# Kernel tuning notes

Hardware: AMD Instinct MI355X
Metric: run time of the kernel (lower is better)

The kernel has to match this reference:

```python
import jax, jax.numpy as jnp
import numpy as np

N_NODES = 50000
N_EDGES = 600000
HIDDEN = 128


def _sage_conv(x, src, dst, W_l, W_r, b):
    """PyG SAGEConv with mean aggregation:
    out_i = W_l @ mean_{j in N(i)} x_j + W_r @ x_i + b
    src/dst: [E] edge endpoints (message flows src -> dst).
    """
    msg = x[src]  # [E, d] gather
    agg = jax.ops.segment_sum(msg, dst, num_segments=N_NODES)  # [N, d]
    cnt = jax.ops.segment_sum(jnp.ones((src.shape[0],), x.dtype), dst,
                              num_segments=N_NODES)  # [N]
    mean = agg / jnp.maximum(cnt, 1.0)[:, None]
    return mean @ W_l.T + x @ W_r.T + b


def setup_inputs() -> dict:
    key = jax.random.key(0)
    ks = jax.random.split(key, 12)
    x = jax.random.normal(ks[0], (N_NODES, HIDDEN), dtype=jnp.float32)
    edge_index = jax.random.randint(ks[1], (2, N_EDGES), 0, N_NODES, dtype=jnp.int64)
    scale = 1.0 / np.sqrt(HIDDEN)
    inp = {"x": x, "edge_index": edge_index}
    for i, layer in enumerate(["1", "2", "3"]):
        inp["Wl" + layer] = jax.random.uniform(ks[2 + 3 * i], (HIDDEN, HIDDEN),
                                               minval=-scale, maxval=scale, dtype=jnp.float32)
        inp["Wr" + layer] = jax.random.uniform(ks[3 + 3 * i], (HIDDEN, HIDDEN),
                                               minval=-scale, maxval=scale, dtype=jnp.float32)
        inp["b" + layer] = jax.random.uniform(ks[4 + 3 * i], (HIDDEN,),
                                              minval=-scale, maxval=scale, dtype=jnp.float32)
    return inp


def reference(x, edge_index, Wl1, Wr1, b1, Wl2, Wr2, b2, Wl3, Wr3, b3):
    src, dst = edge_index[0], edge_index[1]
    h = jax.nn.relu(_sage_conv(x, src, dst, Wl1, Wr1, b1))
    h = _sage_conv(h, src, dst, Wl2, Wr2, b2)
    h = _sage_conv(h, src, dst, Wl3, Wr3, b3)
    return h
```

## Files before the change

kernel.cpp:

```cpp
#include <hip/hip_runtime.h>
#include <hip/hip_bf16.h>

#define N_NODES 50000
#define N_EDGES 600000
#define HID 128

typedef __attribute__((ext_vector_type(8))) short s8v;
typedef __attribute__((ext_vector_type(8))) unsigned short u8v;
typedef __attribute__((ext_vector_type(4))) float f4v;

__device__ __forceinline__ unsigned short f2bf(float x) {
    unsigned u = __float_as_uint(x);
    unsigned r = u + 0x7FFFu + ((u >> 16) & 1u);
    return (unsigned short)(r >> 16);
}
__device__ __forceinline__ float bf2f(unsigned short u) {
    return __uint_as_float((unsigned)u << 16);
}
__device__ __forceinline__ void split_bf(float x, unsigned short& hi, unsigned short& lo) {
    hi = f2bf(x);
    lo = f2bf(x - bf2f(hi));
}

__global__ void detect_mode(const void* __restrict__ edges, int* __restrict__ flag) {
    __shared__ int any;
    if (threadIdx.x == 0) any = 0;
    __syncthreads();
    const int* p = (const int*)edges;
    if (p[2 * threadIdx.x + 1] != 0) any = 1;
    __syncthreads();
    if (threadIdx.x == 0) *flag = (any == 0) ? 1 : 0;
}

__device__ __forceinline__ int edge_at(const void* edges, int mode64, long long idx) {
    return mode64 ? (int)((const long long*)edges)[idx] : ((const int*)edges)[idx];
}

__global__ void count_deg(const void* __restrict__ edges, const int* __restrict__ flag,
                          int* __restrict__ deg) {
    int e = blockIdx.x * 256 + threadIdx.x;
    if (e >= N_EDGES) return;
    int m = *flag;
    int d = edge_at(edges, m, (long long)N_EDGES + e);
    if ((unsigned)d < (unsigned)N_NODES) atomicAdd(&deg[d], 1);
}

__global__ void scan_block(const int* __restrict__ deg, int* __restrict__ offs,
                           int* __restrict__ blocksum) {
    __shared__ int sm[256];
    int i = blockIdx.x * 256 + threadIdx.x;
    int v = (i < N_NODES) ? deg[i] : 0;
    sm[threadIdx.x] = v;
    __syncthreads();
    #pragma unroll
    for (int s = 1; s < 256; s <<= 1) {
        int t = (threadIdx.x >= (unsigned)s) ? sm[threadIdx.x - s] : 0;
        __syncthreads();
        sm[threadIdx.x] += t;
        __syncthreads();
    }
    if (i < N_NODES) offs[i] = sm[threadIdx.x] - v;
    if (threadIdx.x == 255) blocksum[blockIdx.x] = sm[255];
}

__global__ void scan_top(int* __restrict__ blocksum, int nblocks) {
    __shared__ int sm[256];
    int v = ((int)threadIdx.x < nblocks) ? blocksum[threadIdx.x] : 0;
    sm[threadIdx.x] = v;
    __syncthreads();
    #pragma unroll
    for (int s = 1; s < 256; s <<= 1) {
        int t = (threadIdx.x >= (unsigned)s) ? sm[threadIdx.x - s] : 0;
        __syncthreads();
        sm[threadIdx.x] += t;
        __syncthreads();
    }
    if ((int)threadIdx.x < nblocks) blocksum[threadIdx.x] = sm[threadIdx.x] - v;
    if (threadIdx.x == 255) blocksum[nblocks] = sm[255];
}

__global__ void scan_add(int* __restrict__ offs, int* __restrict__ cursor,
                         const int* __restrict__ blocksum, int nblocks) {
    int i = blockIdx.x * 256 + threadIdx.x;
    if (i < N_NODES) {
        int o = offs[i] + blocksum[blockIdx.x];
        offs[i] = o;
        cursor[i] = o;
    }
    if (i == 0) offs[N_NODES] = blocksum[nblocks];
}

__global__ void fill_csr(const void* __restrict__ edges, const int* __restrict__ flag,
                         int* __restrict__ cursor, int* __restrict__ csr) {
    int e = blockIdx.x * 256 + threadIdx.x;
    if (e >= N_EDGES) return;
    int m = *flag;
    int d = edge_at(edges, m, (long long)N_EDGES + e);
    int s = edge_at(edges, m, (long long)e);
    if ((unsigned)d >= (unsigned)N_NODES || (unsigned)s >= (unsigned)N_NODES) return;
    int pos = atomicAdd(&cursor[d], 1);
    csr[pos] = s;
}

__global__ void convert_w(const float* __restrict__ m0, const float* __restrict__ m1,
                          const float* __restrict__ m2, const float* __restrict__ m3,
                          const float* __restrict__ m4, const float* __restrict__ m5,
                          unsigned short* __restrict__ whi, unsigned short* __restrict__ wlo) {
    int idx = blockIdx.x * 256 + threadIdx.x;
    if (idx >= 6 * HID * HID) return;
    int mat = idx >> 14, off = idx & 16383;
    const float* src = mat == 0 ? m0 : mat == 1 ? m1 : mat == 2 ? m2
                     : mat == 3 ? m3 : mat == 4 ? m4 : m5;
    unsigned short h, l;
    split_bf(src[off], h, l);
    whi[idx] = h; wlo[idx] = l;
}

__global__ void split_f32(const float* __restrict__ x, unsigned short* __restrict__ hi,
                          unsigned short* __restrict__ lo, int n4) {
    int i = blockIdx.x * 256 + threadIdx.x;
    if (i >= n4) return;
    float4 v = ((const float4*)x)[i];
    ushort4 h, l;
    split_bf(v.x, h.x, l.x);
    split_bf(v.y, h.y, l.y);
    split_bf(v.z, h.z, l.z);
    split_bf(v.w, h.w, l.w);
    ((ushort4*)hi)[i] = h;
    ((ushort4*)lo)[i] = l;
}

__global__ __launch_bounds__(256) void aggregate_bf16(const unsigned short* __restrict__ h,
                                                      const int* __restrict__ offs,
                                                      const int* __restrict__ csr,
                                                      unsigned short* __restrict__ mhi,
                                                      unsigned short* __restrict__ mlo) {
    const int sub  = threadIdx.x & 15;
    const int node = blockIdx.x * 16 + (threadIdx.x >> 4);
    if (node >= N_NODES) return;
    const int beg = offs[node], end = offs[node + 1];
    float a[8] = {0.f, 0.f, 0.f, 0.f, 0.f, 0.f, 0.f, 0.f};
    int p = beg;
    for (; p + 8 <= end; p += 8) {
        int s0 = csr[p],     s1 = csr[p + 1], s2 = csr[p + 2], s3 = csr[p + 3];
        int s4 = csr[p + 4], s5 = csr[p + 5], s6 = csr[p + 6], s7 = csr[p + 7];
        u8v v0 = *(const u8v*)(h + (size_t)s0 * HID + sub * 8);
        u8v v1 = *(const u8v*)(h + (size_t)s1 * HID + sub * 8);
        u8v v2 = *(const u8v*)(h + (size_t)s2 * HID + sub * 8);
        u8v v3 = *(const u8v*)(h + (size_t)s3 * HID + sub * 8);
        u8v v4 = *(const u8v*)(h + (size_t)s4 * HID + sub * 8);
        u8v v5 = *(const u8v*)(h + (size_t)s5 * HID + sub * 8);
        u8v v6 = *(const u8v*)(h + (size_t)s6 * HID + sub * 8);
        u8v v7 = *(const u8v*)(h + (size_t)s7 * HID + sub * 8);
        #pragma unroll
        for (int j = 0; j < 8; ++j)
            a[j] += ((bf2f(v0[j]) + bf2f(v1[j])) + (bf2f(v2[j]) + bf2f(v3[j])))
                  + ((bf2f(v4[j]) + bf2f(v5[j])) + (bf2f(v6[j]) + bf2f(v7[j])));
    }
    if (p + 4 <= end) {
        int s0 = csr[p], s1 = csr[p + 1], s2 = csr[p + 2], s3 = csr[p + 3];
        u8v v0 = *(const u8v*)(h + (size_t)s0 * HID + sub * 8);
        u8v v1 = *(const u8v*)(h + (size_t)s1 * HID + sub * 8);
        u8v v2 = *(const u8v*)(h + (size_t)s2 * HID + sub * 8);
        u8v v3 = *(const u8v*)(h + (size_t)s3 * HID + sub * 8);
        #pragma unroll
        for (int j = 0; j < 8; ++j)
            a[j] += (bf2f(v0[j]) + bf2f(v1[j])) + (bf2f(v2[j]) + bf2f(v3[j]));
        p += 4;
    }
    for (; p < end; ++p) {
        int s = csr[p];
        u8v v = *(const u8v*)(h + (size_t)s * HID + sub * 8);
        #pragma unroll
        for (int j = 0; j < 8; ++j) a[j] += bf2f(v[j]);
    }
    const float inv = 1.0f / fmaxf((float)(end - beg), 1.0f);
    u8v hh, ll;
    #pragma unroll
    for (int j = 0; j < 8; ++j) {
        unsigned short hj, lj;
        split_bf(a[j] * inv, hj, lj);
        hh[j] = hj; ll[j] = lj;
    }
    *(u8v*)(mhi + (size_t)node * HID + sub * 8) = hh;
    *(u8v*)(mlo + (size_t)node * HID + sub * 8) = ll;
}

template <int RELU, int FINAL>
__global__ __launch_bounds__(256) void sage_mfma(
    const unsigned short* __restrict__ Mhi, const unsigned short* __restrict__ Mlo,
    const unsigned short* __restrict__ Hhi, const unsigned short* __restrict__ Hlo,
    const unsigned short* __restrict__ Whi, const unsigned short* __restrict__ Wlo,
    const float* __restrict__ bias,
    unsigned short* __restrict__ ohi, unsigned short* __restrict__ olo,
    float* __restrict__ of32) {
    __shared__ short BhS[128 * 72];
    __shared__ short BlS[128 * 72];
    const int tid = threadIdx.x;
    const int wave = tid >> 6, lane = tid & 63;
    const int mIdx = lane & 15, q = lane >> 4;
    const int wrow = (wave & 1) * 64, wcol = (wave >> 1) * 64;
    const int rowBase = blockIdx.x * 128;

    size_t aoff[4];
    #pragma unroll
    for (int t = 0; t < 4; ++t) {
        int node = rowBase + wrow + t * 16 + mIdx;
        if (node > N_NODES - 1) node = N_NODES - 1;
        aoff[t] = (size_t)node * HID + q * 8;
    }

    const int bcol = tid & 127;
    const int bseg = (tid >> 7) * 32;

    f4v acc[4][4];
    #pragma unroll
    for (int a = 0; a < 4; ++a)
        #pragma unroll
        for (int b = 0; b < 4; ++b) acc[a][b] = (f4v){0.f, 0.f, 0.f, 0.f};

    s8v Ah[2][4], Al[2][4];
    auto loadA = [&](int i, int buf) {
        const unsigned short* ah_ = (i < 4) ? Mhi : Hhi;
        const unsigned short* al_ = (i < 4) ? Mlo : Hlo;
        const int kc = (i & 3) * 32;
        #pragma unroll
        for (int t = 0; t < 4; ++t) {
            Ah[buf][t] = *(const s8v*)(ah_ + aoff[t] + kc);
            Al[buf][t] = *(const s8v*)(al_ + aoff[t] + kc);
        }
    };

    loadA(0, 0);
    for (int panel = 0; panel < 4; ++panel) {
        const int ph = panel >> 1;
        const int kb = (panel & 1) * 64;
        const unsigned short* Wh_ = Whi + ph * HID * HID;
        const unsigned short* Wl_ = Wlo + ph * HID * HID;
        __syncthreads();
        {
            const unsigned short* sh = Wh_ + bcol * HID + kb + bseg;
            const unsigned short* sl = Wl_ + bcol * HID + kb + bseg;
            short* dh = BhS + bcol * 72 + bseg;
            short* dl = BlS + bcol * 72 + bseg;
            #pragma unroll
            for (int j = 0; j < 4; ++j) {
                *(s8v*)(dh + j * 8) = *(const s8v*)(sh + j * 8);
                *(s8v*)(dl + j * 8) = *(const s8v*)(sl + j * 8);
            }
        }
        __syncthreads();
        #pragma unroll
        for (int c = 0; c < 2; ++c) {
            const int i = panel * 2 + c;
            if (i < 7) loadA(i + 1, (i + 1) & 1);
            const int kc2 = c * 32;
            s8v Bh_f[4], Bl_f[4];
            #pragma unroll
            for (int nt = 0; nt < 4; ++nt) {
                const int a = (wcol + nt * 16 + mIdx) * 72 + kc2 + q * 8;
                Bh_f[nt] = *(const s8v*)(BhS + a);
                Bl_f[nt] = *(const s8v*)(BlS + a);
            }
            const int buf = i & 1;
            #pragma unroll
            for (int mt = 0; mt < 4; ++mt)
                #pragma unroll
                for (int nt = 0; nt < 4; ++nt) {
                    acc[mt][nt] = __builtin_amdgcn_mfma_f32_16x16x32_bf16(
                        Ah[buf][mt], Bh_f[nt], acc[mt][nt], 0, 0, 0);
                    acc[mt][nt] = __builtin_amdgcn_mfma_f32_16x16x32_bf16(
                        Al[buf][mt], Bh_f[nt], acc[mt][nt], 0, 0, 0);
                    acc[mt][nt] = __builtin_amdgcn_mfma_f32_16x16x32_bf16(
                        Ah[buf][mt], Bl_f[nt], acc[mt][nt], 0, 0, 0);
                }
        }
    }

    float bv[4];
    #pragma unroll
    for (int nt = 0; nt < 4; ++nt) bv[nt] = bias[wcol + nt * 16 + mIdx];

    #pragma unroll
    for (int mt = 0; mt < 4; ++mt)
        #pragma unroll
        for (int r = 0; r < 4; ++r) {
            int node = rowBase + wrow + mt * 16 + q * 4 + r;
            if (node < N_NODES) {
                #pragma unroll
                for (int nt = 0; nt < 4; ++nt) {
                    int feat = wcol + nt * 16 + mIdx;
                    float v = acc[mt][nt][r] + bv[nt];
                    if (RELU) v = fmaxf(v, 0.f);
                    size_t oidx = (size_t)node * HID + feat;
                    if (FINAL) {
                        of32[oidx] = v;
                    } else {
                        unsigned short hh, ll;
                        split_bf(v, hh, ll);
                        ohi[oidx] = hh;
                        olo[oidx] = ll;
                    }
                }
            }
        }
}

extern "C" void kernel_launch(void* const* d_in, const int* in_sizes, int n_in,
                              void* d_out, int out_size, void* d_ws, size_t ws_size,
                              hipStream_t stream) {
    const float* x   = (const float*)d_in[0];
    const void* edges = d_in[1];
    const float* Wl1 = (const float*)d_in[2];
    const float* Wr1 = (const float*)d_in[3];
    const float* b1  = (const float*)d_in[4];
    const float* Wl2 = (const float*)d_in[5];
    const float* Wr2 = (const float*)d_in[6];
    const float* b2  = (const float*)d_in[7];
    const float* Wl3 = (const float*)d_in[8];
    const float* Wr3 = (const float*)d_in[9];
    const float* b3  = (const float*)d_in[10];
    float* out = (float*)d_out;

    char* ws = (char*)d_ws;
    size_t off = 0;
    auto alloc = [&](size_t bytes) -> void* {
        void* p = (void*)(ws + off);
        off += (bytes + 255) & ~(size_t)255;
        return p;
    };
    typedef unsigned short u16;
    const size_t FEAT = (size_t)N_NODES * HID;
    int* flag     = (int*)alloc(256);
    int* deg      = (int*)alloc((size_t)N_NODES * 4);
    int* offs     = (int*)alloc((size_t)(N_NODES + 1) * 4);
    int* cursor   = (int*)alloc((size_t)N_NODES * 4);
    int* blocksum = (int*)alloc(256 * 4);
    int* csr      = (int*)alloc((size_t)N_EDGES * 4);
    u16* whi      = (u16*)alloc((size_t)6 * HID * HID * 2);
    u16* wlo      = (u16*)alloc((size_t)6 * HID * HID * 2);
    u16* xhi      = (u16*)alloc(FEAT * 2);
    u16* xlo      = (u16*)alloc(FEAT * 2);
    u16* h1hi     = (u16*)alloc(FEAT * 2);
    u16* h1lo     = (u16*)alloc(FEAT * 2);
    u16* mhi      = (u16*)alloc(FEAT * 2);
    u16* mlo      = (u16*)alloc(FEAT * 2);
    (void)ws_size; (void)in_sizes; (void)n_in; (void)out_size;

    const int EB = (N_EDGES + 255) / 256;
    const int NB = (N_NODES + 255) / 256;
    const int AGG_B = (N_NODES + 15) / 16;
    const int GEMM_B = (N_NODES + 127) / 128;
    const int WCV_B = (6 * HID * HID + 255) / 256;
    const int XSP_B = ((int)(FEAT / 4) + 255) / 256;

    hipMemsetAsync(deg, 0, (size_t)N_NODES * 4, stream);
    detect_mode<<<1, 1024, 0, stream>>>(edges, flag);
    count_deg<<<EB, 256, 0, stream>>>(edges, flag, deg);
    scan_block<<<NB, 256, 0, stream>>>(deg, offs, blocksum);
    scan_top<<<1, 256, 0, stream>>>(blocksum, NB);
    scan_add<<<NB, 256, 0, stream>>>(offs, cursor, blocksum, NB);
    fill_csr<<<EB, 256, 0, stream>>>(edges, flag, cursor, csr);

    convert_w<<<WCV_B, 256, 0, stream>>>(Wl1, Wr1, Wl2, Wr2, Wl3, Wr3, whi, wlo);
    split_f32<<<XSP_B, 256, 0, stream>>>(x, xhi, xlo, (int)(FEAT / 4));

    aggregate_bf16<<<AGG_B, 256, 0, stream>>>(xhi, offs, csr, mhi, mlo);
    sage_mfma<1, 0><<<GEMM_B, 256, 0, stream>>>(mhi, mlo, xhi, xlo,
        whi, wlo, b1, h1hi, h1lo, (float*)nullptr);
    aggregate_bf16<<<AGG_B, 256, 0, stream>>>(h1hi, offs, csr, mhi, mlo);
    sage_mfma<0, 0><<<GEMM_B, 256, 0, stream>>>(mhi, mlo, h1hi, h1lo,
        whi + 2 * HID * HID, wlo + 2 * HID * HID, b2, xhi, xlo, (float*)nullptr);
    aggregate_bf16<<<AGG_B, 256, 0, stream>>>(xhi, offs, csr, mhi, mlo);
    sage_mfma<0, 1><<<GEMM_B, 256, 0, stream>>>(mhi, mlo, xhi, xlo,
        whi + 4 * HID * HID, wlo + 4 * HID * HID, b3,
        (u16*)nullptr, (u16*)nullptr, out);
}
```

Before: 340.7 us.

## Fuse neighbor aggregation into SAGE MFMA layer kernel via shared memory

Each layer now runs one kernel. It first gathers and averages the neighbor features for a 64-node tile straight into shared memory as hi/lo bf16, then runs the MFMA GEMM against the Wl and Wr weights. This drops the global write and re-read of the mean buffers and removes three launches. The weight and x conversion kernels are merged into a single prep launch. In exchange, the tile shrinks from 128 to 64 rows, the K panels get narrower and there are more syncs. The gather phase and the GEMM phase are serialized inside each block, so latency hiding depends on occupancy across blocks.

```diff
diff --git a/kernel.cpp b/kernel.cpp
--- a/kernel.cpp
+++ b/kernel.cpp
@@ -102,179 +102,181 @@
     csr[pos] = s;
 }
 
-__global__ void convert_w(const float* __restrict__ m0, const float* __restrict__ m1,
-                          const float* __restrict__ m2, const float* __restrict__ m3,
-                          const float* __restrict__ m4, const float* __restrict__ m5,
-                          unsigned short* __restrict__ whi, unsigned short* __restrict__ wlo) {
-    int idx = blockIdx.x * 256 + threadIdx.x;
-    if (idx >= 6 * HID * HID) return;
-    int mat = idx >> 14, off = idx & 16383;
-    const float* src = mat == 0 ? m0 : mat == 1 ? m1 : mat == 2 ? m2
-                     : mat == 3 ? m3 : mat == 4 ? m4 : m5;
-    unsigned short h, l;
-    split_bf(src[off], h, l);
-    whi[idx] = h; wlo[idx] = l;
-}
-
-__global__ void split_f32(const float* __restrict__ x, unsigned short* __restrict__ hi,
-                          unsigned short* __restrict__ lo, int n4) {
+__global__ void prep(const float* __restrict__ m0, const float* __restrict__ m1,
+                     const float* __restrict__ m2, const float* __restrict__ m3,
+                     const float* __restrict__ m4, const float* __restrict__ m5,
+                     unsigned short* __restrict__ whi, unsigned short* __restrict__ wlo,
+                     const float* __restrict__ x, unsigned short* __restrict__ xhi,
+                     unsigned short* __restrict__ xlo, int n4) {
     int i = blockIdx.x * 256 + threadIdx.x;
-    if (i >= n4) return;
-    float4 v = ((const float4*)x)[i];
-    ushort4 h, l;
-    split_bf(v.x, h.x, l.x);
-    split_bf(v.y, h.y, l.y);
-    split_bf(v.z, h.z, l.z);
-    split_bf(v.w, h.w, l.w);
-    ((ushort4*)hi)[i] = h;
-    ((ushort4*)lo)[i] = l;
-}
-
-__global__ __launch_bounds__(256) void aggregate_bf16(const unsigned short* __restrict__ h,
-                                                      const int* __restrict__ offs,
-                                                      const int* __restrict__ csr,
-                                                      unsigned short* __restrict__ mhi,
-                                                      unsigned short* __restrict__ mlo) {
-    const int sub  = threadIdx.x & 15;
-    const int node = blockIdx.x * 16 + (threadIdx.x >> 4);
-    if (node >= N_NODES) return;
-    const int beg = offs[node], end = offs[node + 1];
-    float a[8] = {0.f, 0.f, 0.f, 0.f, 0.f, 0.f, 0.f, 0.f};
-    int p = beg;
-    for (; p + 8 <= end; p += 8) {
-        int s0 = csr[p],     s1 = csr[p + 1], s2 = csr[p + 2], s3 = csr[p + 3];
-        int s4 = csr[p + 4], s5 = csr[p + 5], s6 = csr[p + 6], s7 = csr[p + 7];
-        u8v v0 = *(const u8v*)(h + (size_t)s0 * HID + sub * 8);
-        u8v v1 = *(const u8v*)(h + (size_t)s1 * HID + sub * 8);
-        u8v v2 = *(const u8v*)(h + (size_t)s2 * HID + sub * 8);
-        u8v v3 = *(const u8v*)(h + (size_t)s3 * HID + sub * 8);
-        u8v v4 = *(const u8v*)(h + (size_t)s4 * HID + sub * 8);
-        u8v v5 = *(const u8v*)(h + (size_t)s5 * HID + sub * 8);
-        u8v v6 = *(const u8v*)(h + (size_t)s6 * HID + sub * 8);
-        u8v v7 = *(const u8v*)(h + (size_t)s7 * HID + sub * 8);
-        #pragma unroll
-        for (int j = 0; j < 8; ++j)
-            a[j] += ((bf2f(v0[j]) + bf2f(v1[j])) + (bf2f(v2[j]) + bf2f(v3[j])))
-                  + ((bf2f(v4[j]) + bf2f(v5[j])) + (bf2f(v6[j]) + bf2f(v7[j])));
-    }
-    if (p + 4 <= end) {
-        int s0 = csr[p], s1 = csr[p + 1], s2 = csr[p + 2], s3 = csr[p + 3];
-        u8v v0 = *(const u8v*)(h + (size_t)s0 * HID + sub * 8);
-        u8v v1 = *(const u8v*)(h + (size_t)s1 * HID + sub * 8);
-        u8v v2 = *(const u8v*)(h + (size_t)s2 * HID + sub * 8);
-        u8v v3 = *(const u8v*)(h + (size_t)s3 * HID + sub * 8);
-        #pragma unroll
-        for (int j = 0; j < 8; ++j)
-            a[j] += (bf2f(v0[j]) + bf2f(v1[j])) + (bf2f(v2[j]) + bf2f(v3[j]));
-        p += 4;
-    }
-    for (; p < end; ++p) {
-        int s = csr[p];
-        u8v v = *(const u8v*)(h + (size_t)s * HID + sub * 8);
-        #pragma unroll
-        for (int j = 0; j < 8; ++j) a[j] += bf2f(v[j]);
-    }
-    const float inv = 1.0f / fmaxf((float)(end - beg), 1.0f);
-    u8v hh, ll;
-    #pragma unroll
-    for (int j = 0; j < 8; ++j) {
-        unsigned short hj, lj;
-        split_bf(a[j] * inv, hj, lj);
-        hh[j] = hj; ll[j] = lj;
-    }
-    *(u8v*)(mhi + (size_t)node * HID + sub * 8) = hh;
-    *(u8v*)(mlo + (size_t)node * HID + sub * 8) = ll;
+    if (i < 6 * HID * HID) {
+        int mat = i >> 14, off = i & 16383;
+        const float* src = mat == 0 ? m0 : mat == 1 ? m1 : mat == 2 ? m2
+                         : mat == 3 ? m3 : mat == 4 ? m4 : m5;
+        unsigned short h, l;
+        split_bf(src[off], h, l);
+        whi[i] = h; wlo[i] = l;
+    }
+    if (i < n4) {
+        float4 v = ((const float4*)x)[i];
+        ushort4 h, l;
+        split_bf(v.x, h.x, l.x);
+        split_bf(v.y, h.y, l.y);
+        split_bf(v.z, h.z, l.z);
+        split_bf(v.w, h.w, l.w);
+        ((ushort4*)xhi)[i] = h;
+        ((ushort4*)xlo)[i] = l;
+    }
 }
 
 template <int RELU, int FINAL>
-__global__ __launch_bounds__(256) void sage_mfma(
-    const unsigned short* __restrict__ Mhi, const unsigned short* __restrict__ Mlo,
+__global__ __launch_bounds__(256) void sage_layer(
     const unsigned short* __restrict__ Hhi, const unsigned short* __restrict__ Hlo,
+    const int* __restrict__ offs, const int* __restrict__ csr,
     const unsigned short* __restrict__ Whi, const unsigned short* __restrict__ Wlo,
     const float* __restrict__ bias,
     unsigned short* __restrict__ ohi, unsigned short* __restrict__ olo,
     float* __restrict__ of32) {
-    __shared__ short BhS[128 * 72];
-    __shared__ short BlS[128 * 72];
+    __shared__ short MhS[64 * 136];
+    __shared__ short MlS[64 * 136];
+    __shared__ short BhS[128 * 40];
+    __shared__ short BlS[128 * 40];
     const int tid = threadIdx.x;
+    const int rb = blockIdx.x * 64;
+
+    {
+        const int sub = tid & 15;
+        const int grp = tid >> 4;
+        #pragma unroll 1
+        for (int rep = 0; rep < 4; ++rep) {
+            const int nloc = rep * 16 + grp;
+            const int node = rb + nloc;
+            float a[8] = {0.f, 0.f, 0.f, 0.f, 0.f, 0.f, 0.f, 0.f};
+            float inv = 1.0f;
+            if (node < N_NODES) {
+                const int beg = offs[node], end = offs[node + 1];
+                if (end > beg) inv = 1.0f / (float)(end - beg);
+                int p = beg;
+                for (; p + 8 <= end; p += 8) {
+                    int s0 = csr[p],     s1 = csr[p + 1], s2 = csr[p + 2], s3 = csr[p + 3];
+                    int s4 = csr[p + 4], s5 = csr[p + 5], s6 = csr[p + 6], s7 = csr[p + 7];
+                    u8v v0 = *(const u8v*)(Hhi + (size_t)s0 * HID + sub * 8);
+                    u8v v1 = *(const u8v*)(Hhi + (size_t)s1 * HID + sub * 8);
+                    u8v v2 = *(const u8v*)(Hhi + (size_t)s2 * HID + sub * 8);
+                    u8v v3 = *(const u8v*)(Hhi + (size_t)s3 * HID + sub * 8);
+                    u8v v4 = *(const u8v*)(Hhi + (size_t)s4 * HID + sub * 8);
+                    u8v v5 = *(const u8v*)(Hhi + (size_t)s5 * HID + sub * 8);
+                    u8v v6 = *(const u8v*)(Hhi + (size_t)s6 * HID + sub * 8);
+                    u8v v7 = *(const u8v*)(Hhi + (size_t)s7 * HID + sub * 8);
+                    #pragma unroll
+                    for (int j = 0; j < 8; ++j)
+                        a[j] += ((bf2f(v0[j]) + bf2f(v1[j])) + (bf2f(v2[j]) + bf2f(v3[j])))
+                              + ((bf2f(v4[j]) + bf2f(v5[j])) + (bf2f(v6[j]) + bf2f(v7[j])));
+                }
+                if (p + 4 <= end) {
+                    int s0 = csr[p], s1 = csr[p + 1], s2 = csr[p + 2], s3 = csr[p + 3];
+                    u8v v0 = *(const u8v*)(Hhi + (size_t)s0 * HID + sub * 8);
+                    u8v v1 = *(const u8v*)(Hhi + (size_t)s1 * HID + sub * 8);
+                    u8v v2 = *(const u8v*)(Hhi + (size_t)s2 * HID + sub * 8);
+                    u8v v3 = *(const u8v*)(Hhi + (size_t)s3 * HID + sub * 8);
+                    #pragma unroll
+                    for (int j = 0; j < 8; ++j)
+                        a[j] += (bf2f(v0[j]) + bf2f(v1[j])) + (bf2f(v2[j]) + bf2f(v3[j]));
+                    p += 4;
+                }
+                for (; p < end; ++p) {
+                    int s = csr[p];
+                    u8v v = *(const u8v*)(Hhi + (size_t)s * HID + sub * 8);
+                    #pragma unroll
+                    for (int j = 0; j < 8; ++j) a[j] += bf2f(v[j]);
+                }
+            }
+            u8v hh, ll;
+            #pragma unroll
+            for (int j = 0; j < 8; ++j) {
+                unsigned short hj, lj;
+                split_bf(a[j] * inv, hj, lj);
+                hh[j] = hj; ll[j] = lj;
+            }
+            *(u8v*)(&MhS[nloc * 136 + sub * 8]) = hh;
+            *(u8v*)(&MlS[nloc * 136 + sub * 8]) = ll;
+        }
+    }
+
     const int wave = tid >> 6, lane = tid & 63;
     const int mIdx = lane & 15, q = lane >> 4;
-    const int wrow = (wave & 1) * 64, wcol = (wave >> 1) * 64;
-    const int rowBase = blockIdx.x * 128;
-
-    size_t aoff[4];
-    #pragma unroll
-    for (int t = 0; t < 4; ++t) {
-        int node = rowBase + wrow + t * 16 + mIdx;
+    const int wrow = (wave & 1) * 32, wcol = (wave >> 1) * 64;
+
+    size_t aoff[2];
+    #pragma unroll
+    for (int t = 0; t < 2; ++t) {
+        int node = rb + wrow + t * 16 + mIdx;
         if (node > N_NODES - 1) node = N_NODES - 1;
         aoff[t] = (size_t)node * HID + q * 8;
     }
-
     const int bcol = tid & 127;
-    const int bseg = (tid >> 7) * 32;
-
-    f4v acc[4][4];
-    #pragma unroll
-    for (int a = 0; a < 4; ++a)
+    const int bseg = (tid >> 7) * 16;
+
+    f4v acc[2][4];
+    #pragma unroll
+    for (int a = 0; a < 2; ++a)
         #pragma unroll
         for (int b = 0; b < 4; ++b) acc[a][b] = (f4v){0.f, 0.f, 0.f, 0.f};
 
-    s8v Ah[2][4], Al[2][4];
-    auto loadA = [&](int i, int buf) {
-        const unsigned short* ah_ = (i < 4) ? Mhi : Hhi;
-        const unsigned short* al_ = (i < 4) ? Mlo : Hlo;
-        const int kc = (i & 3) * 32;
-        #pragma unroll
-        for (int t = 0; t < 4; ++t) {
-            Ah[buf][t] = *(const s8v*)(ah_ + aoff[t] + kc);
-            Al[buf][t] = *(const s8v*)(al_ + aoff[t] + kc);
-        }
-    };
-
-    loadA(0, 0);
-    for (int panel = 0; panel < 4; ++panel) {
-        const int ph = panel >> 1;
-        const int kb = (panel & 1) * 64;
+    s8v pAh[2][2], pAl[2][2];
+
+    #pragma unroll 1
+    for (int p = 0; p < 8; ++p) {
+        const int ph = p >> 2;
+        const int kb = (p & 3) * 32;
         const unsigned short* Wh_ = Whi + ph * HID * HID;
         const unsigned short* Wl_ = Wlo + ph * HID * HID;
         __syncthreads();
-        {
-            const unsigned short* sh = Wh_ + bcol * HID + kb + bseg;
-            const unsigned short* sl = Wl_ + bcol * HID + kb + bseg;
-            short* dh = BhS + bcol * 72 + bseg;
-            short* dl = BlS + bcol * 72 + bseg;
-            #pragma unroll
-            for (int j = 0; j < 4; ++j) {
-                *(s8v*)(dh + j * 8) = *(const s8v*)(sh + j * 8);
-                *(s8v*)(dl + j * 8) = *(const s8v*)(sl + j * 8);
-            }
-        }
-        __syncthreads();
+        *(s8v*)(&BhS[bcol * 40 + bseg])     = *(const s8v*)(Wh_ + bcol * HID + kb + bseg);
+        *(s8v*)(&BhS[bcol * 40 + bseg + 8]) = *(const s8v*)(Wh_ + bcol * HID + kb + bseg + 8);
+        *(s8v*)(&BlS[bcol * 40 + bseg])     = *(const s8v*)(Wl_ + bcol * HID + kb + bseg);
+        *(s8v*)(&BlS[bcol * 40 + bseg + 8]) = *(const s8v*)(Wl_ + bcol * HID + kb + bseg + 8);
+        __syncthreads();
+        if (p + 1 >= 4 && p + 1 < 8) {
+            const int kc = ((p + 1) & 3) * 32;
+            const int buf = (p + 1) & 1;
+            #pragma unroll
+            for (int t = 0; t < 2; ++t) {
+                pAh[buf][t] = *(const s8v*)(Hhi + aoff[t] + kc);
+                pAl[buf][t] = *(const s8v*)(Hlo + aoff[t] + kc);
+            }
+        }
+        s8v Ah_f[2], Al_f[2];
+        if (p < 4) {
+            #pragma unroll
+            for (int t = 0; t < 2; ++t) {
+                const int r = wrow + t * 16 + mIdx;
+                Ah_f[t] = *(const s8v*)(&MhS[r * 136 + kb + q * 8]);
+                Al_f[t] = *(const s8v*)(&MlS[r * 136 + kb + q * 8]);
+            }
+        } else {
+            const int buf = p & 1;
+            #pragma unroll
+            for (int t = 0; t < 2; ++t) { Ah_f[t] = pAh[buf][t]; Al_f[t] = pAl[buf][t]; }
+        }
+        s8v Bh_f[4], Bl_f[4];
         #pragma unroll
-        for (int c = 0; c < 2; ++c) {
-            const int i = panel * 2 + c;
-            if (i < 7) loadA(i + 1, (i + 1) & 1);
-            const int kc2 = c * 32;
-            s8v Bh_f[4], Bl_f[4];
+        for (int nt = 0; nt < 4; ++nt) {
+            const int a = (wcol + nt * 16 + mIdx) * 40 + q * 8;
+            Bh_f[nt] = *(const s8v*)(&BhS[a]);
+            Bl_f[nt] = *(const s8v*)(&BlS[a]);
+        }
+        #pragma unroll
+        for (int mt = 0; mt < 2; ++mt)
             #pragma unroll
             for (int nt = 0; nt < 4; ++nt) {
-                const int a = (wcol + nt * 16 + mIdx) * 72 + kc2 + q * 8;
-                Bh_f[nt] = *(const s8v*)(BhS + a);
-                Bl_f[nt] = *(const s8v*)(BlS + a);
-            }
-            const int buf = i & 1;
-            #pragma unroll
-            for (int mt = 0; mt < 4; ++mt)
-                #pragma unroll
-                for (int nt = 0; nt < 4; ++nt) {
-                    acc[mt][nt] = __builtin_amdgcn_mfma_f32_16x16x32_bf16(
-                        Ah[buf][mt], Bh_f[nt], acc[mt][nt], 0, 0, 0);
-                    acc[mt][nt] = __builtin_amdgcn_mfma_f32_16x16x32_bf16(
-                        Al[buf][mt], Bh_f[nt], acc[mt][nt], 0, 0, 0);
-                    acc[mt][nt] = __builtin_amdgcn_mfma_f32_16x16x32_bf16(
-                        Ah[buf][mt], Bl_f[nt], acc[mt][nt], 0, 0, 0);
-                }
-        }
+                acc[mt][nt] = __builtin_amdgcn_mfma_f32_16x16x32_bf16(
+                    Ah_f[mt], Bh_f[nt], acc[mt][nt], 0, 0, 0);
+                acc[mt][nt] = __builtin_amdgcn_mfma_f32_16x16x32_bf16(
+                    Al_f[mt], Bh_f[nt], acc[mt][nt], 0, 0, 0);
+                acc[mt][nt] = __builtin_amdgcn_mfma_f32_16x16x32_bf16(
+                    Ah_f[mt], Bl_f[nt], acc[mt][nt], 0, 0, 0);
+            }
     }
 
     float bv[4];
@@ -282,10 +284,10 @@
     for (int nt = 0; nt < 4; ++nt) bv[nt] = bias[wcol + nt * 16 + mIdx];
 
     #pragma unroll
-    for (int mt = 0; mt < 4; ++mt)
+    for (int mt = 0; mt < 2; ++mt)
         #pragma unroll
         for (int r = 0; r < 4; ++r) {
-            int node = rowBase + wrow + mt * 16 + q * 4 + r;
+            int node = rb + wrow + mt * 16 + q * 4 + r;
             if (node < N_NODES) {
                 #pragma unroll
                 for (int nt = 0; nt < 4; ++nt) {
@@ -343,16 +345,12 @@
     u16* xlo      = (u16*)alloc(FEAT * 2);
     u16* h1hi     = (u16*)alloc(FEAT * 2);
     u16* h1lo     = (u16*)alloc(FEAT * 2);
-    u16* mhi      = (u16*)alloc(FEAT * 2);
-    u16* mlo      = (u16*)alloc(FEAT * 2);
     (void)ws_size; (void)in_sizes; (void)n_in; (void)out_size;
 
     const int EB = (N_EDGES + 255) / 256;
     const int NB = (N_NODES + 255) / 256;
-    const int AGG_B = (N_NODES + 15) / 16;
-    const int GEMM_B = (N_NODES + 127) / 128;
-    const int WCV_B = (6 * HID * HID + 255) / 256;
-    const int XSP_B = ((int)(FEAT / 4) + 255) / 256;
+    const int LYR_B = (N_NODES + 63) / 64;
+    const int PREP_B = ((int)(FEAT / 4) + 255) / 256;
 
     hipMemsetAsync(deg, 0, (size_t)N_NODES * 4, stream);
     detect_mode<<<1, 1024, 0, stream>>>(edges, flag);
@@ -361,18 +359,14 @@
     scan_top<<<1, 256, 0, stream>>>(blocksum, NB);
     scan_add<<<NB, 256, 0, stream>>>(offs, cursor, blocksum, NB);
     fill_csr<<<EB, 256, 0, stream>>>(edges, flag, cursor, csr);
-
-    convert_w<<<WCV_B, 256, 0, stream>>>(Wl1, Wr1, Wl2, Wr2, Wl3, Wr3, whi, wlo);
-    split_f32<<<XSP_B, 256, 0, stream>>>(x, xhi, xlo, (int)(FEAT / 4));
-
-    aggregate_bf16<<<AGG_B, 256, 0, stream>>>(xhi, offs, csr, mhi, mlo);
-    sage_mfma<1, 0><<<GEMM_B, 256, 0, stream>>>(mhi, mlo, xhi, xlo,
+    prep<<<PREP_B, 256, 0, stream>>>(Wl1, Wr1, Wl2, Wr2, Wl3, Wr3, whi, wlo,
+                                     x, xhi, xlo, (int)(FEAT / 4));
+
+    sage_layer<1, 0><<<LYR_B, 256, 0, stream>>>(xhi, xlo, offs, csr,
         whi, wlo, b1, h1hi, h1lo, (float*)nullptr);
-    aggregate_bf16<<<AGG_B, 256, 0, stream>>>(h1hi, offs, csr, mhi, mlo);
-    sage_mfma<0, 0><<<GEMM_B, 256, 0, stream>>>(mhi, mlo, h1hi, h1lo,
+    sage_layer<0, 0><<<LYR_B, 256, 0, stream>>>(h1hi, h1lo, offs, csr,
         whi + 2 * HID * HID, wlo + 2 * HID * HID, b2, xhi, xlo, (float*)nullptr);
-    aggregate_bf16<<<AGG_B, 256, 0, stream>>>(xhi, offs, csr, mhi, mlo);
-    sage_mfma<0, 1><<<GEMM_B, 256, 0, stream>>>(mhi, mlo, xhi, xlo,
+    sage_layer<0, 1><<<LYR_B, 256, 0, stream>>>(xhi, xlo, offs, csr,
         whi + 4 * HID * HID, wlo + 4 * HID * HID, b3,
         (u16*)nullptr, (u16*)nullptr, out);
 }
```

Result: slower. 607.4 us (+78.3%).

## Drop low-bf16 part of aggregated means and fuse setup kernels

Applied to the files above, without the earlier changes.

The aggregated mean is now stored only as a single bf16 value, not as a hi/lo pair. This removes the mlo buffer, its writes in aggregation and its reads in the GEMM, and skips one of the three MFMAs for the mean half of K. It also merges the edge-mode detection into count_deg and fill_csr, folds scan_top into scan_add, and fuses weight conversion with feature splitting into one prep kernel. Together these cut kernel launches and memory traffic, at the cost of lower precision in the mean term.

```diff
diff --git a/kernel.cpp b/kernel.cpp
--- a/kernel.cpp
+++ b/kernel.cpp
@@ -22,25 +22,24 @@
     lo = f2bf(x - bf2f(hi));
 }
 
-__global__ void detect_mode(const void* __restrict__ edges, int* __restrict__ flag) {
-    __shared__ int any;
-    if (threadIdx.x == 0) any = 0;
+__device__ __forceinline__ int detect_m64_block(const void* edges) {
+    __shared__ int m64s;
+    if (threadIdx.x == 0) m64s = 1;
     __syncthreads();
     const int* p = (const int*)edges;
-    if (p[2 * threadIdx.x + 1] != 0) any = 1;
+    if (p[2 * threadIdx.x + 1] != 0) m64s = 0;
     __syncthreads();
-    if (threadIdx.x == 0) *flag = (any == 0) ? 1 : 0;
+    return m64s;
 }
 
 __device__ __forceinline__ int edge_at(const void* edges, int mode64, long long idx) {
     return mode64 ? (int)((const long long*)edges)[idx] : ((const int*)edges)[idx];
 }
 
-__global__ void count_deg(const void* __restrict__ edges, const int* __restrict__ flag,
-                          int* __restrict__ deg) {
+__global__ void count_deg(const void* __restrict__ edges, int* __restrict__ deg) {
+    int m = detect_m64_block(edges);
     int e = blockIdx.x * 256 + threadIdx.x;
     if (e >= N_EDGES) return;
-    int m = *flag;
     int d = edge_at(edges, m, (long long)N_EDGES + e);
     if ((unsigned)d < (unsigned)N_NODES) atomicAdd(&deg[d], 1);
 }
@@ -63,7 +62,8 @@
     if (threadIdx.x == 255) blocksum[blockIdx.x] = sm[255];
 }
 
-__global__ void scan_top(int* __restrict__ blocksum, int nblocks) {
+__global__ void scan_add(int* __restrict__ offs, int* __restrict__ cursor,
+                         const int* __restrict__ blocksum, int nblocks) {
     __shared__ int sm[256];
     int v = ((int)threadIdx.x < nblocks) ? blocksum[threadIdx.x] : 0;
     sm[threadIdx.x] = v;
@@ -75,26 +75,22 @@
         sm[threadIdx.x] += t;
         __syncthreads();
     }
-    if ((int)threadIdx.x < nblocks) blocksum[threadIdx.x] = sm[threadIdx.x] - v;
-    if (threadIdx.x == 255) blocksum[nblocks] = sm[255];
-}
-
-__global__ void scan_add(int* __restrict__ offs, int* __restrict__ cursor,
-                         const int* __restrict__ blocksum, int nblocks) {
+    const int pre = (blockIdx.x == 0) ? 0 : sm[blockIdx.x - 1];
+    const int total = sm[nblocks - 1];
     int i = blockIdx.x * 256 + threadIdx.x;
     if (i < N_NODES) {
-        int o = offs[i] + blocksum[blockIdx.x];
+        int o = offs[i] + pre;
         offs[i] = o;
         cursor[i] = o;
     }
-    if (i == 0) offs[N_NODES] = blocksum[nblocks];
-}
-
-__global__ void fill_csr(const void* __restrict__ edges, const int* __restrict__ flag,
-                         int* __restrict__ cursor, int* __restrict__ csr) {
+    if (i == 0) offs[N_NODES] = total;
+}
+
+__global__ void fill_csr(const void* __restrict__ edges, int* __restrict__ cursor,
+                         int* __restrict__ csr) {
+    int m = detect_m64_block(edges);
     int e = blockIdx.x * 256 + threadIdx.x;
     if (e >= N_EDGES) return;
-    int m = *flag;
     int d = edge_at(edges, m, (long long)N_EDGES + e);
     int s = edge_at(edges, m, (long long)e);
     if ((unsigned)d >= (unsigned)N_NODES || (unsigned)s >= (unsigned)N_NODES) return;
@@ -102,39 +98,37 @@
     csr[pos] = s;
 }
 
-__global__ void convert_w(const float* __restrict__ m0, const float* __restrict__ m1,
-                          const float* __restrict__ m2, const float* __restrict__ m3,
-                          const float* __restrict__ m4, const float* __restrict__ m5,
-                          unsigned short* __restrict__ whi, unsigned short* __restrict__ wlo) {
-    int idx = blockIdx.x * 256 + threadIdx.x;
-    if (idx >= 6 * HID * HID) return;
-    int mat = idx >> 14, off = idx & 16383;
-    const float* src = mat == 0 ? m0 : mat == 1 ? m1 : mat == 2 ? m2
-                     : mat == 3 ? m3 : mat == 4 ? m4 : m5;
-    unsigned short h, l;
-    split_bf(src[off], h, l);
-    whi[idx] = h; wlo[idx] = l;
-}
-
-__global__ void split_f32(const float* __restrict__ x, unsigned short* __restrict__ hi,
-                          unsigned short* __restrict__ lo, int n4) {
+__global__ void prep(const float* __restrict__ m0, const float* __restrict__ m1,
+                     const float* __restrict__ m2, const float* __restrict__ m3,
+                     const float* __restrict__ m4, const float* __restrict__ m5,
+                     unsigned short* __restrict__ whi, unsigned short* __restrict__ wlo,
+                     const float* __restrict__ x, unsigned short* __restrict__ xhi,
+                     unsigned short* __restrict__ xlo, int n4) {
     int i = blockIdx.x * 256 + threadIdx.x;
-    if (i >= n4) return;
-    float4 v = ((const float4*)x)[i];
-    ushort4 h, l;
-    split_bf(v.x, h.x, l.x);
-    split_bf(v.y, h.y, l.y);
-    split_bf(v.z, h.z, l.z);
-    split_bf(v.w, h.w, l.w);
-    ((ushort4*)hi)[i] = h;
-    ((ushort4*)lo)[i] = l;
+    if (i < 6 * HID * HID) {
+        int mat = i >> 14, off = i & 16383;
+        const float* src = mat == 0 ? m0 : mat == 1 ? m1 : mat == 2 ? m2
+                         : mat == 3 ? m3 : mat == 4 ? m4 : m5;
+        unsigned short h, l;
+        split_bf(src[off], h, l);
+        whi[i] = h; wlo[i] = l;
+    }
+    if (i < n4) {
+        float4 v = ((const float4*)x)[i];
+        ushort4 h, l;
+        split_bf(v.x, h.x, l.x);
+        split_bf(v.y, h.y, l.y);
+        split_bf(v.z, h.z, l.z);
+        split_bf(v.w, h.w, l.w);
+        ((ushort4*)xhi)[i] = h;
+        ((ushort4*)xlo)[i] = l;
+    }
 }
 
 __global__ __launch_bounds__(256) void aggregate_bf16(const unsigned short* __restrict__ h,
                                                       const int* __restrict__ offs,
                                                       const int* __restrict__ csr,
-                                                      unsigned short* __restrict__ mhi,
-                                                      unsigned short* __restrict__ mlo) {
+                                                      unsigned short* __restrict__ mhi) {
     const int sub  = threadIdx.x & 15;
     const int node = blockIdx.x * 16 + (threadIdx.x >> 4);
     if (node >= N_NODES) return;
@@ -175,20 +169,15 @@
         for (int j = 0; j < 8; ++j) a[j] += bf2f(v[j]);
     }
     const float inv = 1.0f / fmaxf((float)(end - beg), 1.0f);
-    u8v hh, ll;
-    #pragma unroll
-    for (int j = 0; j < 8; ++j) {
-        unsigned short hj, lj;
-        split_bf(a[j] * inv, hj, lj);
-        hh[j] = hj; ll[j] = lj;
-    }
+    u8v hh;
+    #pragma unroll
+    for (int j = 0; j < 8; ++j) hh[j] = f2bf(a[j] * inv);
     *(u8v*)(mhi + (size_t)node * HID + sub * 8) = hh;
-    *(u8v*)(mlo + (size_t)node * HID + sub * 8) = ll;
 }
 
 template <int RELU, int FINAL>
 __global__ __launch_bounds__(256) void sage_mfma(
-    const unsigned short* __restrict__ Mhi, const unsigned short* __restrict__ Mlo,
+    const unsigned short* __restrict__ Mhi,
     const unsigned short* __restrict__ Hhi, const unsigned short* __restrict__ Hlo,
     const unsigned short* __restrict__ Whi, const unsigned short* __restrict__ Wlo,
     const float* __restrict__ bias,
@@ -209,7 +198,6 @@
         if (node > N_NODES - 1) node = N_NODES - 1;
         aoff[t] = (size_t)node * HID + q * 8;
     }
-
     const int bcol = tid & 127;
     const int bseg = (tid >> 7) * 32;
 
@@ -221,17 +209,22 @@
 
     s8v Ah[2][4], Al[2][4];
     auto loadA = [&](int i, int buf) {
-        const unsigned short* ah_ = (i < 4) ? Mhi : Hhi;
-        const unsigned short* al_ = (i < 4) ? Mlo : Hlo;
         const int kc = (i & 3) * 32;
-        #pragma unroll
-        for (int t = 0; t < 4; ++t) {
-            Ah[buf][t] = *(const s8v*)(ah_ + aoff[t] + kc);
-            Al[buf][t] = *(const s8v*)(al_ + aoff[t] + kc);
+        if (i < 4) {
+            #pragma unroll
+            for (int t = 0; t < 4; ++t)
+                Ah[buf][t] = *(const s8v*)(Mhi + aoff[t] + kc);
+        } else {
+            #pragma unroll
+            for (int t = 0; t < 4; ++t) {
+                Ah[buf][t] = *(const s8v*)(Hhi + aoff[t] + kc);
+                Al[buf][t] = *(const s8v*)(Hlo + aoff[t] + kc);
+            }
         }
     };
 
     loadA(0, 0);
+    #pragma unroll 1
     for (int panel = 0; panel < 4; ++panel) {
         const int ph = panel >> 1;
         const int kb = (panel & 1) * 64;
@@ -263,17 +256,29 @@
                 Bl_f[nt] = *(const s8v*)(BlS + a);
             }
             const int buf = i & 1;
-            #pragma unroll
-            for (int mt = 0; mt < 4; ++mt)
+            if (panel < 2) {
                 #pragma unroll
-                for (int nt = 0; nt < 4; ++nt) {
-                    acc[mt][nt] = __builtin_amdgcn_mfma_f32_16x16x32_bf16(
-                        Ah[buf][mt], Bh_f[nt], acc[mt][nt], 0, 0, 0);
-                    acc[mt][nt] = __builtin_amdgcn_mfma_f32_16x16x32_bf16(
-                        Al[buf][mt], Bh_f[nt], acc[mt][nt], 0, 0, 0);
-                    acc[mt][nt] = __builtin_amdgcn_mfma_f32_16x16x32_bf16(
-                        Ah[buf][mt], Bl_f[nt], acc[mt][nt], 0, 0, 0);
-                }
+                for (int mt = 0; mt < 4; ++mt)
+                    #pragma unroll
+                    for (int nt = 0; nt < 4; ++nt) {
+                        acc[mt][nt] = __builtin_amdgcn_mfma_f32_16x16x32_bf16(
+                            Ah[buf][mt], Bh_f[nt], acc[mt][nt], 0, 0, 0);
+                        acc[mt][nt] = __builtin_amdgcn_mfma_f32_16x16x32_bf16(
+                            Ah[buf][mt], Bl_f[nt], acc[mt][nt], 0, 0, 0);
+                    }
+            } else {
+                #pragma unroll
+                for (int mt = 0; mt < 4; ++mt)
+                    #pragma unroll
+                    for (int nt = 0; nt < 4; ++nt) {
+                        acc[mt][nt] = __builtin_amdgcn_mfma_f32_16x16x32_bf16(
+                            Ah[buf][mt], Bh_f[nt], acc[mt][nt], 0, 0, 0);
+                        acc[mt][nt] = __builtin_amdgcn_mfma_f32_16x16x32_bf16(
+                            Al[buf][mt], Bh_f[nt], acc[mt][nt], 0, 0, 0);
+                        acc[mt][nt] = __builtin_amdgcn_mfma_f32_16x16x32_bf16(
+                            Ah[buf][mt], Bl_f[nt], acc[mt][nt], 0, 0, 0);
+                    }
+            }
         }
     }
 
@@ -331,7 +336,6 @@
     };
     typedef unsigned short u16;
     const size_t FEAT = (size_t)N_NODES * HID;
-    int* flag     = (int*)alloc(256);
     int* deg      = (int*)alloc((size_t)N_NODES * 4);
     int* offs     = (int*)alloc((size_t)(N_NODES + 1) * 4);
     int* cursor   = (int*)alloc((size_t)N_NODES * 4);
@@ -344,35 +348,30 @@
     u16* h1hi     = (u16*)alloc(FEAT * 2);
     u16* h1lo     = (u16*)alloc(FEAT * 2);
     u16* mhi      = (u16*)alloc(FEAT * 2);
-    u16* mlo      = (u16*)alloc(FEAT * 2);
     (void)ws_size; (void)in_sizes; (void)n_in; (void)out_size;
 
     const int EB = (N_EDGES + 255) / 256;
     const int NB = (N_NODES + 255) / 256;
     const int AGG_B = (N_NODES + 15) / 16;
     const int GEMM_B = (N_NODES + 127) / 128;
-    const int WCV_B = (6 * HID * HID + 255) / 256;
-    const int XSP_B = ((int)(FEAT / 4) + 255) / 256;
+    const int PREP_B = ((int)(FEAT / 4) + 255) / 256;
 
     hipMemsetAsync(deg, 0, (size_t)N_NODES * 4, stream);
-    detect_mode<<<1, 1024, 0, stream>>>(edges, flag);
-    count_deg<<<EB, 256, 0, stream>>>(edges, flag, deg);
+    count_deg<<<EB, 256, 0, stream>>>(edges, deg);
     scan_block<<<NB, 256, 0, stream>>>(deg, offs, blocksum);
-    scan_top<<<1, 256, 0, stream>>>(blocksum, NB);
     scan_add<<<NB, 256, 0, stream>>>(offs, cursor, blocksum, NB);
-    fill_csr<<<EB, 256, 0, stream>>>(edges, flag, cursor, csr);
-
-    convert_w<<<WCV_B, 256, 0, stream>>>(Wl1, Wr1, Wl2, Wr2, Wl3, Wr3, whi, wlo);
-    split_f32<<<XSP_B, 256, 0, stream>>>(x, xhi, xlo, (int)(FEAT / 4));
-
-    aggregate_bf16<<<AGG_B, 256, 0, stream>>>(xhi, offs, csr, mhi, mlo);
-    sage_mfma<1, 0><<<GEMM_B, 256, 0, stream>>>(mhi, mlo, xhi, xlo,
+    fill_csr<<<EB, 256, 0, stream>>>(edges, cursor, csr);
+    prep<<<PREP_B, 256, 0, stream>>>(Wl1, Wr1, Wl2, Wr2, Wl3, Wr3, whi, wlo,
+                                     x, xhi, xlo, (int)(FEAT / 4));
+
+    aggregate_bf16<<<AGG_B, 256, 0, stream>>>(xhi, offs, csr, mhi);
+    sage_mfma<1, 0><<<GEMM_B, 256, 0, stream>>>(mhi, xhi, xlo,
         whi, wlo, b1, h1hi, h1lo, (float*)nullptr);
-    aggregate_bf16<<<AGG_B, 256, 0, stream>>>(h1hi, offs, csr, mhi, mlo);
-    sage_mfma<0, 0><<<GEMM_B, 256, 0, stream>>>(mhi, mlo, h1hi, h1lo,
+    aggregate_bf16<<<AGG_B, 256, 0, stream>>>(h1hi, offs, csr, mhi);
+    sage_mfma<0, 0><<<GEMM_B, 256, 0, stream>>>(mhi, h1hi, h1lo,
         whi + 2 * HID * HID, wlo + 2 * HID * HID, b2, xhi, xlo, (float*)nullptr);
-    aggregate_bf16<<<AGG_B, 256, 0, stream>>>(xhi, offs, csr, mhi, mlo);
-    sage_mfma<0, 1><<<GEMM_B, 256, 0, stream>>>(mhi, mlo, xhi, xlo,
+    aggregate_bf16<<<AGG_B, 256, 0, stream>>>(xhi, offs, csr, mhi);
+    sage_mfma<0, 1><<<GEMM_B, 256, 0, stream>>>(mhi, xhi, xlo,
         whi + 4 * HID * HID, wlo + 4 * HID * HID, b3,
         (u16*)nullptr, (u16*)nullptr, out);
 }
```

Measured after the change: 356.1 us. +4.5%, slower.
